# Optimization experiments

Hardware: AMD Instinct MI355X
Metric: run time of the kernel (lower is better)

The kernel has to match this reference:

```python
import jax, jax.numpy as jnp
import numpy as np

HEADS = 16
LN_EPS = 1e-5


def setup_inputs() -> dict:
    key = jax.random.key(0)
    ks = jax.random.split(key, 8)
    B, S, D = 2, 2048, 1024
    F = 4 * D
    std = 0.02
    return {
        "x": jax.random.normal(ks[0], (B, S, D), jnp.float32),
        # QKV projections (stored as (in, out)); kaiming-normal-like scale
        "Wq": jax.random.normal(ks[1], (D, D), jnp.float32) * std,
        "bq": jnp.zeros((D,), jnp.float32),
        "Wk": jax.random.normal(ks[2], (D, D), jnp.float32) * std,
        "bk": jnp.zeros((D,), jnp.float32),
        "Wv": jax.random.normal(ks[3], (D, D), jnp.float32) * std,
        "bv": jnp.zeros((D,), jnp.float32),
        # FFN
        "W1": jax.random.normal(ks[4], (D, F), jnp.float32) * std,
        "b1": jnp.zeros((F,), jnp.float32),
        "W2": jax.random.normal(ks[5], (F, D), jnp.float32) * std,
        "b2": jnp.zeros((D,), jnp.float32),
        # LayerNorm
        "gamma": jnp.ones((D,), jnp.float32),
        "beta": jnp.zeros((D,), jnp.float32),
    }


def reference(x, Wq, bq, Wk, bk, Wv, bv, W1, b1, W2, b2, gamma, beta):
    B, S, D = x.shape
    H = HEADS
    hd = D // H
    # QKV projections -> [B, H, S, hd]
    Q = (x @ Wq + bq).reshape(B, S, H, hd).transpose(0, 2, 1, 3)
    K = (x @ Wk + bk).reshape(B, S, H, hd).transpose(0, 2, 1, 3)
    V = (x @ Wv + bv).reshape(B, S, H, hd).transpose(0, 2, 1, 3)
    # scores scaled by sqrt(embedding_dim), faithful to source (not head_dim)
    scores = jnp.einsum('bhqd,bhkd->bhqk', Q, K) / jnp.sqrt(jnp.asarray(D, x.dtype))
    attn = jax.nn.softmax(scores, axis=-1)
    # diagonal_training: zero the diagonal of the post-softmax attention matrix
    attn = attn * (1.0 - jnp.eye(S, dtype=attn.dtype))
    out = jnp.einsum('bhqk,bhkd->bhqd', attn, V)
    out = out.transpose(0, 2, 1, 3).reshape(B, S, D)
    # dropout is identity in eval mode
    h = jax.nn.gelu(out @ W1 + b1, approximate=False) @ W2 + b2
    # LayerNorm
    mu = jnp.mean(h, axis=-1, keepdims=True)
    var = jnp.var(h, axis=-1, keepdims=True)
    return (h - mu) * jax.lax.rsqrt(var + LN_EPS) * gamma + beta
```

## Files before the change

### kernel.cpp

```cpp
#include <hip/hip_runtime.h>

using bf16x8 = __attribute__((ext_vector_type(8))) short;
using f32x4  = __attribute__((ext_vector_type(4))) float;

__device__ __forceinline__ float b2f(ushort u) {
  union { unsigned int i; float f; } v; v.i = ((unsigned int)u) << 16; return v.f;
}
__device__ __forceinline__ ushort f2b(float f) {
  unsigned int x = __float_as_uint(f);
  unsigned int r = (x + 0x7FFFu + ((x >> 16) & 1u)) >> 16;
  return (ushort)r;
}
__device__ __forceinline__ unsigned cvt_pk_bf16(float a, float b) {
  unsigned r;
  asm("v_cvt_pk_bf16_f32 %0, %1, %2" : "=v"(r) : "v"(a), "v"(b));
  return r;
}

__device__ __forceinline__ void gld_lds16(const void* g, void* l) {
  __builtin_amdgcn_global_load_lds(
      (const __attribute__((address_space(1))) void*)g,
      (__attribute__((address_space(3))) void*)l, 16, 0, 0);
}


__global__ void cast_bf16_kernel(const float* __restrict__ in, ushort* __restrict__ out, int n) {
  int i = (blockIdx.x * blockDim.x + threadIdx.x) * 4;
  if (i < n) {
    float4 v = *(const float4*)(in + i);
    ushort4 o = make_ushort4(f2b(v.x), f2b(v.y), f2b(v.z), f2b(v.w));
    *(ushort4*)(out + i) = o;
  }
}

__global__ void transpose_cast_qkv_kernel(const float* __restrict__ Wq,
                                          const float* __restrict__ Wk,
                                          const float* __restrict__ Wv,
                                          ushort* __restrict__ out) {
  __shared__ float tile[32][33];
  const float* in = (blockIdx.z == 0) ? Wq : (blockIdx.z == 1) ? Wk : Wv;
  ushort* dst = out + (size_t)blockIdx.z * 1024 * 1024;
  int tx = threadIdx.x, ty = threadIdx.y;
  int cb = blockIdx.x * 32, rb = blockIdx.y * 32;
  for (int i = ty; i < 32; i += 8)
    tile[i][tx] = in[(size_t)(rb + i) * 1024 + (cb + tx)];
  __syncthreads();
  for (int i = ty; i < 32; i += 8)
    dst[(size_t)(cb + i) * 1024 + (rb + tx)] = f2b(tile[tx][i]);
}

__global__ void transpose_cast_ffn_kernel(const float* __restrict__ W1, ushort* __restrict__ W1t,
                                          const float* __restrict__ W2, ushort* __restrict__ W2t) {
  __shared__ float tile[32][33];
  int t = blockIdx.x;
  const float* in; ushort* out; int R, C, cb, rb;
  if (t < 4096) { in = W1; out = W1t; R = 1024; C = 4096; cb = (t & 127) * 32; rb = (t >> 7) * 32; }
  else { t -= 4096; in = W2; out = W2t; R = 4096; C = 1024; cb = (t & 31) * 32; rb = (t >> 5) * 32; }
  int tx = threadIdx.x, ty = threadIdx.y;
  for (int i = ty; i < 32; i += 8)
    tile[i][tx] = in[(size_t)(rb + i) * C + (cb + tx)];
  __syncthreads();
  for (int i = ty; i < 32; i += 8)
    out[(size_t)(cb + i) * R + (rb + tx)] = f2b(tile[tx][i]);
}

__global__ void transpose_v_kernel(const ushort* __restrict__ V, ushort* __restrict__ Vt) {
  __shared__ ushort t[32][33];
  int bh = blockIdx.z;
  int b = bh >> 4, h = bh & 15;
  int s0 = blockIdx.x * 32, d0 = blockIdx.y * 32;
  const ushort* Vbp = V + ((size_t)b * 2048) * 1024 + h * 64;
  ushort* Vtb = Vt + (size_t)bh * 64 * 2048;
  int tx = threadIdx.x, ty = threadIdx.y;
  for (int i = ty; i < 32; i += 8) t[i][tx] = Vbp[(size_t)(s0 + i) * 1024 + d0 + tx];
  __syncthreads();
  for (int i = ty; i < 32; i += 8) Vtb[(size_t)(d0 + i) * 2048 + s0 + tx] = t[tx][i];
}


template<int EPI>
__global__ __launch_bounds__(256) void gemm128(
    const ushort* __restrict__ A, const ushort* __restrict__ Bt,
    const float* __restrict__ bias, void* __restrict__ Cout,
    int M, int N, int K)
{
  __shared__ ushort Asm_[2][128 * 32];
  __shared__ ushort Bsm_[2][128 * 32];

  const int nwg = gridDim.x * gridDim.y;
  const int bid = blockIdx.y * gridDim.x + blockIdx.x;
  const int cpx = nwg >> 3;
  const int swz = (bid & 7) * cpx + (bid >> 3);
  const int bm = (swz % gridDim.x) * 128;
  const int bn = (swz / gridDim.x) * 128;

  const int tid = threadIdx.x;
  const int lane = tid & 63, w = tid >> 6;
  const int wm = (w >> 1) * 64, wn = (w & 1) * 64;
  const int g = lane >> 4, c = lane & 15;
  const int swz8 = ((g ^ ((c >> 1) & 3)) * 8);
  const int srow = tid >> 2;
  const int scol = (((tid & 3) ^ ((srow >> 1) & 3)) * 8);
  const int soff = srow * 32 + (tid & 3) * 8;

  const ushort* gA0 = A  + (size_t)(bm + srow) * K + scol;
  const ushort* gA1 = gA0 + (size_t)64 * K;
  const ushort* gB0 = Bt + (size_t)(bn + srow) * K + scol;
  const ushort* gB1 = gB0 + (size_t)64 * K;

  f32x4 acc[4][4] = {};
  const int nt = K / 32;

  gld_lds16(gA0, &Asm_[0][soff]);
  gld_lds16(gA1, &Asm_[0][64 * 32 + soff]);
  gld_lds16(gB0, &Bsm_[0][soff]);
  gld_lds16(gB1, &Bsm_[0][64 * 32 + soff]);
  __syncthreads();

  int cur = 0;
  for (int t = 0; t < nt; ++t) {
    if (t + 1 < nt) {
      int k0 = (t + 1) * 32;
      gld_lds16(gA0 + k0, &Asm_[cur ^ 1][soff]);
      gld_lds16(gA1 + k0, &Asm_[cur ^ 1][64 * 32 + soff]);
      gld_lds16(gB0 + k0, &Bsm_[cur ^ 1][soff]);
      gld_lds16(gB1 + k0, &Bsm_[cur ^ 1][64 * 32 + soff]);
    }
    bf16x8 af[4], bfr[4];
    #pragma unroll
    for (int m = 0; m < 4; ++m)
      af[m] = *(const bf16x8*)&Asm_[cur][(wm + m * 16 + c) * 32 + swz8];
    #pragma unroll
    for (int n = 0; n < 4; ++n)
      bfr[n] = *(const bf16x8*)&Bsm_[cur][(wn + n * 16 + c) * 32 + swz8];
    __builtin_amdgcn_s_setprio(1);
    #pragma unroll
    for (int m = 0; m < 4; ++m)
      #pragma unroll
      for (int n = 0; n < 4; ++n)
        acc[m][n] = __builtin_amdgcn_mfma_f32_16x16x32_bf16(af[m], bfr[n], acc[m][n], 0, 0, 0);
    __builtin_amdgcn_s_setprio(0);
    __syncthreads();
    cur ^= 1;
  }

  ushort* eb = (ushort*)Asm_ + w * 1088;
  const int er = lane >> 3;
  const int es = (lane & 7) * 8;
  float bia[4];
  #pragma unroll
  for (int n = 0; n < 4; ++n) bia[n] = bias[bn + wn + n * 16 + c];

  #pragma unroll
  for (int mf = 0; mf < 4; ++mf) {
    #pragma unroll
    for (int n = 0; n < 4; ++n) {
      #pragma unroll
      for (int r = 0; r < 4; ++r) {
        float v = acc[mf][n][r] + bia[n];
        if (EPI == 1) {
          float u = 0.7978845608028654f * (v + 0.044715f * v * v * v);
          float au = fabsf(u);
          float e = __expf(-2.0f * au);
          float th = (1.0f - e) / (1.0f + e);
          th = copysignf(th, u);
          v = 0.5f * v * (1.0f + th);
        }
        eb[(g * 4 + r) * 68 + n * 16 + c] = f2b(v);
      }
    }
    asm volatile("" ::: "memory");
    bf16x8 v0 = *(const bf16x8*)&eb[er * 68 + es];
    bf16x8 v1 = *(const bf16x8*)&eb[(er + 8) * 68 + es];
    int grow = bm + wm + mf * 16 + er;
    int gcol = bn + wn + es;
    if (EPI == 3) {
      ushort* dst = (ushort*)Cout + (size_t)(gcol >> 10) * 4194304 + (gcol & 1023);
      *(bf16x8*)(dst + (size_t)grow * 1024) = v0;
      *(bf16x8*)(dst + (size_t)(grow + 8) * 1024) = v1;
    } else {
      ushort* dst = (ushort*)Cout + gcol;
      *(bf16x8*)(dst + (size_t)grow * N) = v0;
      *(bf16x8*)(dst + (size_t)(grow + 8) * N) = v1;
    }
    asm volatile("" ::: "memory");
  }
}


template<int EPI>
__global__ __launch_bounds__(512) void gemm256(
    const ushort* __restrict__ A, const ushort* __restrict__ Bt,
    const float* __restrict__ bias, void* __restrict__ Cout,
    int M, int N, int K)
{
  extern __shared__ ushort lds[];

  const int nwg = gridDim.x * gridDim.y;
  const int bid = blockIdx.y * gridDim.x + blockIdx.x;
  const int cpx = nwg >> 3;
  const int swz = (bid & 7) * cpx + (bid >> 3);
  const int bm = (swz % gridDim.x) * 256;
  const int bn = (swz / gridDim.x) * 256;

  const int tid = threadIdx.x;
  const int lane = tid & 63, w = tid >> 6;
  const int wr = w >> 2, wc = w & 3;
  const int hi = lane >> 4, c = lane & 15;

  const int srow0 = tid >> 3;
  const int scolx = (((tid & 7) ^ (srow0 & 7)) * 8);
  const ushort* gA = A  + (size_t)(bm + srow0) * K + scolx;
  const ushort* gB = Bt + (size_t)(bn + srow0) * K + scolx;

  const int NT = K / 64;
  f32x4 acc[8][4] = {};

  auto STAGE = [&](int buf, int t) {
    ushort* bA = lds + buf * 32768;
    ushort* bB = bA + 16384;
    const size_t ko = (size_t)t * 64;
    #pragma unroll
    for (int ch = 0; ch < 4; ++ch) {
      gld_lds16(gA + (size_t)ch * 64 * K + ko, bA + ch * 4096 + tid * 8);
      gld_lds16(gB + (size_t)ch * 64 * K + ko, bB + ch * 4096 + tid * 8);
    }
  };

  STAGE(0, 0);
  __syncthreads();

  int cur = 0;
  for (int t = 0; t < NT; ++t) {
    if (t + 1 < NT) STAGE(cur ^ 1, t + 1);
    const ushort* sA = lds + cur * 32768;
    const ushort* sB = sA + 16384;
    #pragma unroll
    for (int kk = 0; kk < 2; ++kk) {
      bf16x8 bf[4], af[8];
      #pragma unroll
      for (int n = 0; n < 4; ++n) {
        int row = wc * 64 + n * 16 + c;
        bf[n] = *(const bf16x8*)&sB[row * 64 + (((kk * 4 + hi) ^ (c & 7)) * 8)];
      }
      #pragma unroll
      for (int m = 0; m < 8; ++m) {
        int row = wr * 128 + m * 16 + c;
        af[m] = *(const bf16x8*)&sA[row * 64 + (((kk * 4 + hi) ^ (c & 7)) * 8)];
      }
      __builtin_amdgcn_s_setprio(1);
      #pragma unroll
      for (int m = 0; m < 8; ++m)
        #pragma unroll
        for (int n = 0; n < 4; ++n)
          acc[m][n] = __builtin_amdgcn_mfma_f32_16x16x32_bf16(af[m], bf[n], acc[m][n], 0, 0, 0);
      __builtin_amdgcn_s_setprio(0);
    }
    __syncthreads();
    cur ^= 1;
  }

  ushort* eb = &lds[w * 1088];
  const int g = hi;
  const int er = lane >> 3;
  const int es = (lane & 7) * 8;
  float bia[4];
  #pragma unroll
  for (int n = 0; n < 4; ++n) bia[n] = bias[bn + wc * 64 + n * 16 + c];

  #pragma unroll
  for (int mf = 0; mf < 8; ++mf) {
    #pragma unroll
    for (int n = 0; n < 4; ++n) {
      #pragma unroll
      for (int r = 0; r < 4; ++r) {
        float v = acc[mf][n][r] + bia[n];
        if (EPI == 1) {
          float u = 0.7978845608028654f * (v + 0.044715f * v * v * v);
          float au = fabsf(u);
          float e = __expf(-2.0f * au);
          float th = (1.0f - e) / (1.0f + e);
          th = copysignf(th, u);
          v = 0.5f * v * (1.0f + th);
        }
        eb[(g * 4 + r) * 68 + n * 16 + c] = f2b(v);
      }
    }
    asm volatile("" ::: "memory");
    bf16x8 v0 = *(const bf16x8*)&eb[er * 68 + es];
    bf16x8 v1 = *(const bf16x8*)&eb[(er + 8) * 68 + es];
    int grow = bm + wr * 128 + mf * 16 + er;
    int gcol = bn + wc * 64 + es;
    if (EPI == 3) {
      ushort* dst = (ushort*)Cout + (size_t)(gcol >> 10) * 4194304 + (gcol & 1023);
      *(bf16x8*)(dst + (size_t)grow * 1024) = v0;
      *(bf16x8*)(dst + (size_t)(grow + 8) * 1024) = v1;
    } else {
      ushort* dst = (ushort*)Cout + gcol;
      *(bf16x8*)(dst + (size_t)grow * N) = v0;
      *(bf16x8*)(dst + (size_t)(grow + 8) * N) = v1;
    }
    asm volatile("" ::: "memory");
  }
}


#define BM 128
#define BN 128
#define BK 32

__global__ __launch_bounds__(256) void gemm_bf16_f32(
    const ushort* __restrict__ A, const ushort* __restrict__ Bt,
    float* __restrict__ C0, float* __restrict__ C1,
    float* __restrict__ C2, float* __restrict__ C3,
    int M, int N, int Kstride, int k_len)
{
  __shared__ ushort Asm_[2][BM * BK];
  __shared__ ushort Bsm_[2][BN * BK];
  const int bm = blockIdx.x * BM, bn = blockIdx.y * BN;
  const int k_begin = blockIdx.z * k_len;
  const int tid = threadIdx.x;
  const int lane = tid & 63, w = tid >> 6;
  const int wm = (w >> 1) * 64, wn = (w & 1) * 64;
  const int g = lane >> 4, c = lane & 15;
  const int swz8 = ((g ^ ((c >> 1) & 3)) * 8);
  const int srow = tid >> 2;
  const int scol = (((tid & 3) ^ ((srow >> 1) & 3)) * 8);
  const int soff = srow * 32 + (tid & 3) * 8;

  const ushort* gA0 = A  + (size_t)(bm + srow) * Kstride + k_begin + scol;
  const ushort* gA1 = gA0 + (size_t)64 * Kstride;
  const ushort* gB0 = Bt + (size_t)(bn + srow) * Kstride + k_begin + scol;
  const ushort* gB1 = gB0 + (size_t)64 * Kstride;

  f32x4 acc[4][4] = {};
  const int nt = k_len / BK;

  gld_lds16(gA0, &Asm_[0][soff]);
  gld_lds16(gA1, &Asm_[0][64 * 32 + soff]);
  gld_lds16(gB0, &Bsm_[0][soff]);
  gld_lds16(gB1, &Bsm_[0][64 * 32 + soff]);
  __syncthreads();

  int cur = 0;
  for (int t = 0; t < nt; ++t) {
    if (t + 1 < nt) {
      int k0 = (t + 1) * BK;
      gld_lds16(gA0 + k0, &Asm_[cur ^ 1][soff]);
      gld_lds16(gA1 + k0, &Asm_[cur ^ 1][64 * 32 + soff]);
      gld_lds16(gB0 + k0, &Bsm_[cur ^ 1][soff]);
      gld_lds16(gB1 + k0, &Bsm_[cur ^ 1][64 * 32 + soff]);
    }
    bf16x8 af[4], bfr[4];
    #pragma unroll
    for (int m = 0; m < 4; ++m)
      af[m] = *(const bf16x8*)&Asm_[cur][(wm + m * 16 + c) * 32 + swz8];
    #pragma unroll
    for (int n = 0; n < 4; ++n)
      bfr[n] = *(const bf16x8*)&Bsm_[cur][(wn + n * 16 + c) * 32 + swz8];
    #pragma unroll
    for (int m = 0; m < 4; ++m)
      #pragma unroll
      for (int n = 0; n < 4; ++n)
        acc[m][n] = __builtin_amdgcn_mfma_f32_16x16x32_bf16(af[m], bfr[n], acc[m][n], 0, 0, 0);
    __syncthreads();
    cur ^= 1;
  }

  float* dst = C0;
  if (blockIdx.z == 1) dst = C1;
  else if (blockIdx.z == 2) dst = C2;
  else if (blockIdx.z == 3) dst = C3;

  #pragma unroll
  for (int n = 0; n < 4; ++n) {
    int col = bn + wn + n * 16 + c;
    #pragma unroll
    for (int m = 0; m < 4; ++m)
      #pragma unroll
      for (int r = 0; r < 4; ++r) {
        int row = bm + wm + m * 16 + g * 4 + r;
        dst[(size_t)row * N + col] = acc[m][n][r];
      }
  }
}


#define ATT_SC2 0.0450842202f

__global__ __launch_bounds__(512) void attn_kernel(
    const ushort* __restrict__ Q, const ushort* __restrict__ K,
    const ushort* __restrict__ V, const ushort* __restrict__ Vt,
    ushort* __restrict__ Out)
{
  const int bid = blockIdx.x;
  const int tile = (bid & 7) * 64 + (bid >> 3);
  const int bh = tile >> 4;
  const int q0 = (tile & 15) * 128;
  const int b = bh >> 4, h = bh & 15;
  const int tid = threadIdx.x;
  const int w = tid >> 6, lane = tid & 63;
  const int hi = lane >> 4, c = lane & 15;
  const int qw = q0 + w * 16;

  const size_t boff = ((size_t)b * 2048) * 1024 + h * 64;
  const ushort* Qp = Q + boff;
  const ushort* Kp = K + boff;
  const ushort* Vp = V + boff;
  const ushort* Vtb = Vt + (size_t)bh * 64 * 2048;

  __shared__ ushort Ksm[2][64 * 64];
  __shared__ ushort Vsm[2][64 * 64];
  __shared__ ushort Psm[8][16 * 72];

  const int srow = tid >> 3;
  const int sslot = tid & 7;
  const int scolx = ((sslot ^ (srow & 7)) * 8);
  const ushort* gK = Kp + (size_t)srow * 1024 + scolx;
  const ushort* gV = Vtb + (size_t)srow * 2048 + scolx;

  bf16x8 qf0 = *(const bf16x8*)(Qp + (size_t)(qw + c) * 1024 + hi * 8);
  bf16x8 qf1 = *(const bf16x8*)(Qp + (size_t)(qw + c) * 1024 + 32 + hi * 8);
  {
    ushort* q0p = (ushort*)&qf0;
    ushort* q1p = (ushort*)&qf1;
    #pragma unroll
    for (int j = 0; j < 8; ++j) {
      q0p[j] = f2b(b2f(q0p[j]) * ATT_SC2);
      q1p[j] = f2b(b2f(q1p[j]) * ATT_SC2);
    }
  }

  f32x4 acc[4] = {};
  float l_run = 0.f;

  gld_lds16(gK, &Ksm[0][tid * 8]);
  gld_lds16(gV, &Vsm[0][tid * 8]);
  __syncthreads();

  const int nt = 2048 / 64;
  for (int t = 0; t < nt; ++t) {
    const int buf = t & 1;
    if (t + 1 < nt) {
      gld_lds16(gK + (size_t)(t + 1) * 64 * 1024, &Ksm[buf ^ 1][tid * 8]);
      gld_lds16(gV + (size_t)(t + 1) * 64,        &Vsm[buf ^ 1][tid * 8]);
    }

    f32x4 sv[4];
    __builtin_amdgcn_s_setprio(1);
    #pragma unroll
    for (int sub = 0; sub < 4; ++sub) {
      int rr = sub * 16 + c;
      int sw = (rr & 7) * 8;
      bf16x8 k0 = *(const bf16x8*)&Ksm[buf][rr * 64 + ((hi * 8) ^ sw)];
      bf16x8 k1 = *(const bf16x8*)&Ksm[buf][rr * 64 + ((32 + hi * 8) ^ sw)];
      f32x4 z = {};
      z = __builtin_amdgcn_mfma_f32_16x16x32_bf16(k0, qf0, z, 0, 0, 0);
      z = __builtin_amdgcn_mfma_f32_16x16x32_bf16(k1, qf1, z, 0, 0, 0);
      sv[sub] = z;
    }
    __builtin_amdgcn_s_setprio(0);

    float p[16];
    float psum = 0.f;
    #pragma unroll
    for (int sub = 0; sub < 4; ++sub)
      #pragma unroll
      for (int r = 0; r < 4; ++r) { float e = exp2f(sv[sub][r]); p[sub * 4 + r] = e; psum += e; }
    psum += __shfl_xor(psum, 16);
    psum += __shfl_xor(psum, 32);
    l_run += psum;

    #pragma unroll
    for (int sub = 0; sub < 4; ++sub) {
      uint2 pk;
      pk.x = cvt_pk_bf16(p[sub * 4 + 0], p[sub * 4 + 1]);
      pk.y = cvt_pk_bf16(p[sub * 4 + 2], p[sub * 4 + 3]);
      *(uint2*)&Psm[w][c * 72 + sub * 16 + hi * 4] = pk;
    }
    asm volatile("" ::: "memory");

    bf16x8 pa0 = *(const bf16x8*)&Psm[w][c * 72 + hi * 8];
    bf16x8 pa1 = *(const bf16x8*)&Psm[w][c * 72 + 32 + hi * 8];
    __builtin_amdgcn_s_setprio(1);
    #pragma unroll
    for (int dsub = 0; dsub < 4; ++dsub) {
      int rr = dsub * 16 + c;
      int sw = (rr & 7) * 8;
      bf16x8 v0 = *(const bf16x8*)&Vsm[buf][rr * 64 + ((hi * 8) ^ sw)];
      bf16x8 v1 = *(const bf16x8*)&Vsm[buf][rr * 64 + ((32 + hi * 8) ^ sw)];
      acc[dsub] = __builtin_amdgcn_mfma_f32_16x16x32_bf16(pa0, v0, acc[dsub], 0, 0, 0);
      acc[dsub] = __builtin_amdgcn_mfma_f32_16x16x32_bf16(pa1, v1, acc[dsub], 0, 0, 0);
    }
    __builtin_amdgcn_s_setprio(0);

    __syncthreads();
  }

  #pragma unroll
  for (int r = 0; r < 4; ++r) {
    int q = qw + hi * 4 + r;
    float part = 0.f;
    #pragma unroll
    for (int t = 0; t < 4; ++t)
      part += b2f(Qp[(size_t)q * 1024 + c * 4 + t]) * b2f(Kp[(size_t)q * 1024 + c * 4 + t]);
    #pragma unroll
    for (int off = 1; off < 16; off <<= 1) part += __shfl_xor(part, off);
    float lq = __shfl(l_run, hi * 4 + r, 16);
    float pqq = exp2f(part * ATT_SC2);
    float inv = 1.f / lq;
    #pragma unroll
    for (int dsub = 0; dsub < 4; ++dsub) {
      float vq = b2f(Vp[(size_t)q * 1024 + dsub * 16 + c]);
      float o = (acc[dsub][r] - pqq * vq) * inv;
      Out[((size_t)(b * 2048 + q) * 16 + h) * 64 + dsub * 16 + c] = f2b(o);
    }
  }
}


__global__ __launch_bounds__(256) void ln_kernel(float* __restrict__ h,
                                                 const float* __restrict__ p1,
                                                 const float* __restrict__ p2,
                                                 const float* __restrict__ p3,
                                                 const float* __restrict__ b2,
                                                 const float* __restrict__ gamma,
                                                 const float* __restrict__ beta, int np) {
  int row = blockIdx.x, tid = threadIdx.x;
  float* hr = h + (size_t)row * 1024;
  float4 v = ((const float4*)hr)[tid];
  float4 p = ((const float4*)(p1 + (size_t)row * 1024))[tid];
  float4 bb = ((const float4*)b2)[tid];
  v.x += p.x + bb.x; v.y += p.y + bb.y; v.z += p.z + bb.z; v.w += p.w + bb.w;
  if (np == 4) {
    float4 a = ((const float4*)(p2 + (size_t)row * 1024))[tid];
    float4 d = ((const float4*)(p3 + (size_t)row * 1024))[tid];
    v.x += a.x + d.x; v.y += a.y + d.y; v.z += a.z + d.z; v.w += a.w + d.w;
  }
  float s = v.x + v.y + v.z + v.w;
  #pragma unroll
  for (int off = 1; off < 64; off <<= 1) s += __shfl_xor(s, off);
  __shared__ float red[2][4];
  int wv = tid >> 6, lane = tid & 63;
  if (lane == 0) red[0][wv] = s;
  __syncthreads();
  float mu = (red[0][0] + red[0][1] + red[0][2] + red[0][3]) * (1.0f / 1024.0f);
  float dx = v.x - mu, dy = v.y - mu, dz = v.z - mu, dw = v.w - mu;
  float q = dx * dx + dy * dy + dz * dz + dw * dw;
  #pragma unroll
  for (int off = 1; off < 64; off <<= 1) q += __shfl_xor(q, off);
  if (lane == 0) red[1][wv] = q;
  __syncthreads();
  float var = (red[1][0] + red[1][1] + red[1][2] + red[1][3]) * (1.0f / 1024.0f);
  float is = rsqrtf(var + 1e-5f);
  float4 gm = ((const float4*)gamma)[tid];
  float4 bt = ((const float4*)beta)[tid];
  float4 o;
  o.x = dx * is * gm.x + bt.x;
  o.y = dy * is * gm.y + bt.y;
  o.z = dz * is * gm.z + bt.z;
  o.w = dw * is * gm.w + bt.w;
  ((float4*)hr)[tid] = o;
}


extern "C" void kernel_launch(void* const* d_in, const int* in_sizes, int n_in,
                              void* d_out, int out_size, void* d_ws, size_t ws_size,
                              hipStream_t stream) {
  const float* x  = (const float*)d_in[0];
  const float* Wq = (const float*)d_in[1];
  const float* bq = (const float*)d_in[2];
  const float* Wk = (const float*)d_in[3];
  const float* bk = (const float*)d_in[4];
  const float* Wv = (const float*)d_in[5];
  const float* bv = (const float*)d_in[6];
  const float* W1 = (const float*)d_in[7];
  const float* b1 = (const float*)d_in[8];
  const float* W2 = (const float*)d_in[9];
  const float* b2 = (const float*)d_in[10];
  const float* gamma = (const float*)d_in[11];
  const float* beta  = (const float*)d_in[12];
  float* out = (float*)d_out;

  char* ws = (char*)d_ws;
  const size_t MB = 1u << 20;
  ushort* xb    = (ushort*)(ws + 0);
  ushort* Wqkvt = (ushort*)(ws + 8 * MB);
  ushort* Qb    = (ushort*)(ws + 14 * MB);
  ushort* Kb    = (ushort*)(ws + 22 * MB);
  ushort* Vb    = (ushort*)(ws + 30 * MB);
  ushort* Vt    = (ushort*)(ws + 38 * MB);
  ushort* AO    = (ushort*)(ws + 46 * MB);
  ushort* W1t   = (ushort*)(ws + 54 * MB);
  ushort* h1    = (ushort*)(ws + 0);
  ushort* W2t   = (ushort*)(ws + 32 * MB);
  float*  p1    = (float*)(ws + 40 * MB);
  float*  p2    = (float*)(ws + 56 * MB);
  float*  p3    = (float*)(ws + 72 * MB);
  float*  bqkv  = (float*)(ws + 46 * MB);

  const bool split4 = (ws_size >= (size_t)89 * MB);

  (void)hipMemcpyAsync(bqkv,        bq, 4096, hipMemcpyDeviceToDevice, stream);
  (void)hipMemcpyAsync(bqkv + 1024, bk, 4096, hipMemcpyDeviceToDevice, stream);
  (void)hipMemcpyAsync(bqkv + 2048, bv, 4096, hipMemcpyDeviceToDevice, stream);

  dim3 tb(32, 8);
  cast_bf16_kernel<<<4096, 256, 0, stream>>>(x, xb, 4194304);
  transpose_cast_qkv_kernel<<<dim3(32, 32, 3), tb, 0, stream>>>(Wq, Wk, Wv, Wqkvt);

  gemm128<3><<<dim3(32, 24), 256, 0, stream>>>(xb, Wqkvt, bqkv, Qb, 4096, 3072, 1024);

  transpose_v_kernel<<<dim3(64, 2, 32), tb, 0, stream>>>(Vb, Vt);

  attn_kernel<<<512, 512, 0, stream>>>(Qb, Kb, Vb, Vt, AO);

  transpose_cast_ffn_kernel<<<8192, tb, 0, stream>>>(W1, W1t, W2, W2t);

  gemm256<1><<<dim3(16, 16), 512, 131072, stream>>>(AO, W1t, b1, h1, 4096, 4096, 1024);

  if (split4) {
    gemm_bf16_f32<<<dim3(32, 8, 4), 256, 0, stream>>>(h1, W2t, out, p1, p2, p3,
                                                      4096, 1024, 4096, 1024);
    ln_kernel<<<4096, 256, 0, stream>>>(out, p1, p2, p3, b2, gamma, beta, 4);
  } else {
    gemm_bf16_f32<<<dim3(32, 8, 2), 256, 0, stream>>>(h1, W2t, out, p1, nullptr, nullptr,
                                                      4096, 1024, 4096, 2048);
    ln_kernel<<<4096, 256, 0, stream>>>(out, p1, nullptr, nullptr, b2, gamma, beta, 2);
  }
}
```

Before: 234.5 us.

## Swap GEMM tile shapes: 256x256 tiles for QKV, 128x128 BK64 tiles for FFN1

The QKV projection now uses the 256x256, 512-thread kernel with 128KB dynamic LDS (192 workgroups). The FFN1 GEMM moves to a new 128x128 tile kernel with BK=64 and an XOR-swizzled LDS layout (1024 workgroups). Both kernels drop the workgroup-ID swizzle for L2 locality and the s_setprio hints. This rebalances tile count against CU count and data reuse, but QKV's 192 workgroups may underfill the GPU and the loss of the L2 swizzle may add cache misses.

```diff
diff --git a/kernel.cpp b/kernel.cpp
--- a/kernel.cpp
+++ b/kernel.cpp
@@ -79,80 +79,81 @@
 
 
 template<int EPI>
-__global__ __launch_bounds__(256) void gemm128(
+__global__ __launch_bounds__(512) void gemm256(
     const ushort* __restrict__ A, const ushort* __restrict__ Bt,
     const float* __restrict__ bias, void* __restrict__ Cout,
     int M, int N, int K)
 {
-  __shared__ ushort Asm_[2][128 * 32];
-  __shared__ ushort Bsm_[2][128 * 32];
-
-  const int nwg = gridDim.x * gridDim.y;
-  const int bid = blockIdx.y * gridDim.x + blockIdx.x;
-  const int cpx = nwg >> 3;
-  const int swz = (bid & 7) * cpx + (bid >> 3);
-  const int bm = (swz % gridDim.x) * 128;
-  const int bn = (swz / gridDim.x) * 128;
+  extern __shared__ ushort lds[];
+
+  const int bm = blockIdx.x * 256;
+  const int bn = blockIdx.y * 256;
 
   const int tid = threadIdx.x;
   const int lane = tid & 63, w = tid >> 6;
-  const int wm = (w >> 1) * 64, wn = (w & 1) * 64;
-  const int g = lane >> 4, c = lane & 15;
-  const int swz8 = ((g ^ ((c >> 1) & 3)) * 8);
-  const int srow = tid >> 2;
-  const int scol = (((tid & 3) ^ ((srow >> 1) & 3)) * 8);
-  const int soff = srow * 32 + (tid & 3) * 8;
-
-  const ushort* gA0 = A  + (size_t)(bm + srow) * K + scol;
-  const ushort* gA1 = gA0 + (size_t)64 * K;
-  const ushort* gB0 = Bt + (size_t)(bn + srow) * K + scol;
-  const ushort* gB1 = gB0 + (size_t)64 * K;
-
-  f32x4 acc[4][4] = {};
-  const int nt = K / 32;
-
-  gld_lds16(gA0, &Asm_[0][soff]);
-  gld_lds16(gA1, &Asm_[0][64 * 32 + soff]);
-  gld_lds16(gB0, &Bsm_[0][soff]);
-  gld_lds16(gB1, &Bsm_[0][64 * 32 + soff]);
+  const int wr = w >> 2, wc = w & 3;
+  const int hi = lane >> 4, c = lane & 15;
+
+  const int srow0 = tid >> 3;
+  const int scolx = (((tid & 7) ^ (srow0 & 7)) * 8);
+  const ushort* gA = A  + (size_t)(bm + srow0) * K + scolx;
+  const ushort* gB = Bt + (size_t)(bn + srow0) * K + scolx;
+
+  const int NT = K / 64;
+  f32x4 acc[8][4] = {};
+
+  auto STAGE = [&](int buf, int t) {
+    ushort* bA = lds + buf * 32768;
+    ushort* bB = bA + 16384;
+    const size_t ko = (size_t)t * 64;
+    #pragma unroll
+    for (int ch = 0; ch < 4; ++ch) {
+      gld_lds16(gA + (size_t)ch * 64 * K + ko, bA + ch * 4096 + tid * 8);
+      gld_lds16(gB + (size_t)ch * 64 * K + ko, bB + ch * 4096 + tid * 8);
+    }
+  };
+
+  STAGE(0, 0);
   __syncthreads();
 
   int cur = 0;
-  for (int t = 0; t < nt; ++t) {
-    if (t + 1 < nt) {
-      int k0 = (t + 1) * 32;
-      gld_lds16(gA0 + k0, &Asm_[cur ^ 1][soff]);
-      gld_lds16(gA1 + k0, &Asm_[cur ^ 1][64 * 32 + soff]);
-      gld_lds16(gB0 + k0, &Bsm_[cur ^ 1][soff]);
-      gld_lds16(gB1 + k0, &Bsm_[cur ^ 1][64 * 32 + soff]);
-    }
-    bf16x8 af[4], bfr[4];
-    #pragma unroll
-    for (int m = 0; m < 4; ++m)
-      af[m] = *(const bf16x8*)&Asm_[cur][(wm + m * 16 + c) * 32 + swz8];
-    #pragma unroll
-    for (int n = 0; n < 4; ++n)
-      bfr[n] = *(const bf16x8*)&Bsm_[cur][(wn + n * 16 + c) * 32 + swz8];
-    __builtin_amdgcn_s_setprio(1);
-    #pragma unroll
-    for (int m = 0; m < 4; ++m)
-      #pragma unroll
-      for (int n = 0; n < 4; ++n)
-        acc[m][n] = __builtin_amdgcn_mfma_f32_16x16x32_bf16(af[m], bfr[n], acc[m][n], 0, 0, 0);
-    __builtin_amdgcn_s_setprio(0);
+  for (int t = 0; t < NT; ++t) {
+    if (t + 1 < NT) STAGE(cur ^ 1, t + 1);
+    const ushort* sA = lds + cur * 32768;
+    const ushort* sB = sA + 16384;
+    #pragma unroll
+    for (int kk = 0; kk < 2; ++kk) {
+      bf16x8 bf[4], af[8];
+      #pragma unroll
+      for (int n = 0; n < 4; ++n) {
+        int row = wc * 64 + n * 16 + c;
+        bf[n] = *(const bf16x8*)&sB[row * 64 + (((kk * 4 + hi) ^ (c & 7)) * 8)];
+      }
+      #pragma unroll
+      for (int m = 0; m < 8; ++m) {
+        int row = wr * 128 + m * 16 + c;
+        af[m] = *(const bf16x8*)&sA[row * 64 + (((kk * 4 + hi) ^ (c & 7)) * 8)];
+      }
+      #pragma unroll
+      for (int m = 0; m < 8; ++m)
+        #pragma unroll
+        for (int n = 0; n < 4; ++n)
+          acc[m][n] = __builtin_amdgcn_mfma_f32_16x16x32_bf16(af[m], bf[n], acc[m][n], 0, 0, 0);
+    }
     __syncthreads();
     cur ^= 1;
   }
 
-  ushort* eb = (ushort*)Asm_ + w * 1088;
+  ushort* eb = &lds[w * 1088];
+  const int g = hi;
   const int er = lane >> 3;
   const int es = (lane & 7) * 8;
   float bia[4];
   #pragma unroll
-  for (int n = 0; n < 4; ++n) bia[n] = bias[bn + wn + n * 16 + c];
-
-  #pragma unroll
-  for (int mf = 0; mf < 4; ++mf) {
+  for (int n = 0; n < 4; ++n) bia[n] = bias[bn + wc * 64 + n * 16 + c];
+
+  #pragma unroll
+  for (int mf = 0; mf < 8; ++mf) {
     #pragma unroll
     for (int n = 0; n < 4; ++n) {
       #pragma unroll
@@ -172,8 +173,8 @@
     asm volatile("" ::: "memory");
     bf16x8 v0 = *(const bf16x8*)&eb[er * 68 + es];
     bf16x8 v1 = *(const bf16x8*)&eb[(er + 8) * 68 + es];
-    int grow = bm + wm + mf * 16 + er;
-    int gcol = bn + wn + es;
+    int grow = bm + wr * 128 + mf * 16 + er;
+    int gcol = bn + wc * 64 + es;
     if (EPI == 3) {
       ushort* dst = (ushort*)Cout + (size_t)(gcol >> 10) * 4194304 + (gcol & 1023);
       *(bf16x8*)(dst + (size_t)grow * 1024) = v0;
@@ -189,41 +190,36 @@
 
 
 template<int EPI>
-__global__ __launch_bounds__(512) void gemm256(
+__global__ __launch_bounds__(256) void gemm128x64(
     const ushort* __restrict__ A, const ushort* __restrict__ Bt,
     const float* __restrict__ bias, void* __restrict__ Cout,
     int M, int N, int K)
 {
-  extern __shared__ ushort lds[];
-
-  const int nwg = gridDim.x * gridDim.y;
-  const int bid = blockIdx.y * gridDim.x + blockIdx.x;
-  const int cpx = nwg >> 3;
-  const int swz = (bid & 7) * cpx + (bid >> 3);
-  const int bm = (swz % gridDim.x) * 256;
-  const int bn = (swz / gridDim.x) * 256;
+  __shared__ ushort Asm_[2][128 * 64];
+  __shared__ ushort Bsm_[2][128 * 64];
+
+  const int bm = blockIdx.x * 128;
+  const int bn = blockIdx.y * 128;
 
   const int tid = threadIdx.x;
   const int lane = tid & 63, w = tid >> 6;
-  const int wr = w >> 2, wc = w & 3;
+  const int wm = (w >> 1) * 64, wn = (w & 1) * 64;
   const int hi = lane >> 4, c = lane & 15;
 
-  const int srow0 = tid >> 3;
-  const int scolx = (((tid & 7) ^ (srow0 & 7)) * 8);
-  const ushort* gA = A  + (size_t)(bm + srow0) * K + scolx;
-  const ushort* gB = Bt + (size_t)(bn + srow0) * K + scolx;
+  const int srow = tid >> 3;
+  const int scolx = (((tid & 7) ^ (srow & 7)) * 8);
+  const ushort* gA = A  + (size_t)(bm + srow) * K + scolx;
+  const ushort* gB = Bt + (size_t)(bn + srow) * K + scolx;
 
   const int NT = K / 64;
-  f32x4 acc[8][4] = {};
+  f32x4 acc[4][4] = {};
 
   auto STAGE = [&](int buf, int t) {
-    ushort* bA = lds + buf * 32768;
-    ushort* bB = bA + 16384;
     const size_t ko = (size_t)t * 64;
     #pragma unroll
     for (int ch = 0; ch < 4; ++ch) {
-      gld_lds16(gA + (size_t)ch * 64 * K + ko, bA + ch * 4096 + tid * 8);
-      gld_lds16(gB + (size_t)ch * 64 * K + ko, bB + ch * 4096 + tid * 8);
+      gld_lds16(gA + (size_t)ch * 32 * K + ko, &Asm_[buf][ch * 2048 + tid * 8]);
+      gld_lds16(gB + (size_t)ch * 32 * K + ko, &Bsm_[buf][ch * 2048 + tid * 8]);
     }
   };
 
@@ -233,43 +229,39 @@
   int cur = 0;
   for (int t = 0; t < NT; ++t) {
     if (t + 1 < NT) STAGE(cur ^ 1, t + 1);
-    const ushort* sA = lds + cur * 32768;
-    const ushort* sB = sA + 16384;
     #pragma unroll
     for (int kk = 0; kk < 2; ++kk) {
-      bf16x8 bf[4], af[8];
+      bf16x8 af[4], bfr[4];
+      #pragma unroll
+      for (int m = 0; m < 4; ++m) {
+        int row = wm + m * 16 + c;
+        af[m] = *(const bf16x8*)&Asm_[cur][row * 64 + (((kk * 4 + hi) ^ (c & 7)) * 8)];
+      }
       #pragma unroll
       for (int n = 0; n < 4; ++n) {
-        int row = wc * 64 + n * 16 + c;
-        bf[n] = *(const bf16x8*)&sB[row * 64 + (((kk * 4 + hi) ^ (c & 7)) * 8)];
+        int row = wn + n * 16 + c;
+        bfr[n] = *(const bf16x8*)&Bsm_[cur][row * 64 + (((kk * 4 + hi) ^ (c & 7)) * 8)];
       }
       #pragma unroll
-      for (int m = 0; m < 8; ++m) {
-        int row = wr * 128 + m * 16 + c;
-        af[m] = *(const bf16x8*)&sA[row * 64 + (((kk * 4 + hi) ^ (c & 7)) * 8)];
-      }
-      __builtin_amdgcn_s_setprio(1);
-      #pragma unroll
-      for (int m = 0; m < 8; ++m)
+      for (int m = 0; m < 4; ++m)
         #pragma unroll
         for (int n = 0; n < 4; ++n)
-          acc[m][n] = __builtin_amdgcn_mfma_f32_16x16x32_bf16(af[m], bf[n], acc[m][n], 0, 0, 0);
-      __builtin_amdgcn_s_setprio(0);
+          acc[m][n] = __builtin_amdgcn_mfma_f32_16x16x32_bf16(af[m], bfr[n], acc[m][n], 0, 0, 0);
     }
     __syncthreads();
     cur ^= 1;
   }
 
-  ushort* eb = &lds[w * 1088];
+  ushort* eb = (ushort*)Asm_ + w * 1088;
   const int g = hi;
   const int er = lane >> 3;
   const int es = (lane & 7) * 8;
   float bia[4];
   #pragma unroll
-  for (int n = 0; n < 4; ++n) bia[n] = bias[bn + wc * 64 + n * 16 + c];
-
-  #pragma unroll
-  for (int mf = 0; mf < 8; ++mf) {
+  for (int n = 0; n < 4; ++n) bia[n] = bias[bn + wn + n * 16 + c];
+
+  #pragma unroll
+  for (int mf = 0; mf < 4; ++mf) {
     #pragma unroll
     for (int n = 0; n < 4; ++n) {
       #pragma unroll
@@ -289,8 +281,8 @@
     asm volatile("" ::: "memory");
     bf16x8 v0 = *(const bf16x8*)&eb[er * 68 + es];
     bf16x8 v1 = *(const bf16x8*)&eb[(er + 8) * 68 + es];
-    int grow = bm + wr * 128 + mf * 16 + er;
-    int gcol = bn + wc * 64 + es;
+    int grow = bm + wm + mf * 16 + er;
+    int gcol = bn + wn + es;
     if (EPI == 3) {
       ushort* dst = (ushort*)Cout + (size_t)(gcol >> 10) * 4194304 + (gcol & 1023);
       *(bf16x8*)(dst + (size_t)grow * 1024) = v0;
@@ -609,7 +601,7 @@
   cast_bf16_kernel<<<4096, 256, 0, stream>>>(x, xb, 4194304);
   transpose_cast_qkv_kernel<<<dim3(32, 32, 3), tb, 0, stream>>>(Wq, Wk, Wv, Wqkvt);
 
-  gemm128<3><<<dim3(32, 24), 256, 0, stream>>>(xb, Wqkvt, bqkv, Qb, 4096, 3072, 1024);
+  gemm256<3><<<dim3(16, 12), 512, 131072, stream>>>(xb, Wqkvt, bqkv, Qb, 4096, 3072, 1024);
 
   transpose_v_kernel<<<dim3(64, 2, 32), tb, 0, stream>>>(Vb, Vt);
 
@@ -617,7 +609,7 @@
 
   transpose_cast_ffn_kernel<<<8192, tb, 0, stream>>>(W1, W1t, W2, W2t);
 
-  gemm256<1><<<dim3(16, 16), 512, 131072, stream>>>(AO, W1t, b1, h1, 4096, 4096, 1024);
+  gemm128x64<1><<<dim3(32, 32), 256, 0, stream>>>(AO, W1t, b1, h1, 4096, 4096, 1024);
 
   if (split4) {
     gemm_bf16_f32<<<dim3(32, 8, 4), 256, 0, stream>>>(h1, W2t, out, p1, p2, p3,
```

New measurement: 239.0 us. No clear change (+1.9%).
